# Kernel optimization log

Measured on AMD Instinct MI355X. Metric: run time of the kernel, lower is better.

Reference implementation:

```python
import jax, jax.numpy as jnp
from jax import lax
import numpy as np

# db3 analysis/synthesis filter bank (pywt coefficients)
DEC_LO = np.array([0.035226291882100656, -0.085441273882241486, -0.13501102001039084,
                   0.45987750211933132, 0.80689150931333875, 0.33267055295095688], dtype=np.float32)
DEC_HI = np.array([-0.33267055295095688, 0.80689150931333875, -0.45987750211933132,
                   -0.13501102001039084, 0.085441273882241486, 0.035226291882100656], dtype=np.float32)
REC_LO = DEC_LO[::-1].copy()
REC_HI = np.array([0.035226291882100656, 0.085441273882241486, -0.13501102001039084,
                   -0.45987750211933132, 0.80689150931333875, -0.33267055295095688], dtype=np.float32)
L = 6  # db3 filter length
DN = ('NCHW', 'OIHW', 'NCHW')

# analysis correlation kernels (torch conv2d correlates, pytorch_wavelets pre-flips dec filters)
H0_A = jnp.asarray(DEC_LO[::-1].copy())
H1_A = jnp.asarray(DEC_HI[::-1].copy())
# synthesis: conv_transpose(x, g, stride=2, pad=L-2) == correlate(dilate(x,2), flip(g), pad=1)
G0_S = jnp.asarray(REC_LO[::-1].copy())
G1_S = jnp.asarray(REC_HI[::-1].copy())


def _sep_conv(x, f, axis, stride=1, lhs_dil=1, pad=0):
    """Depthwise 1-D correlation along H (axis=2) or W (axis=3) of an NCHW tensor."""
    C = x.shape[1]
    if axis == 2:
        k = jnp.tile(f.reshape(1, 1, -1, 1), (C, 1, 1, 1))
        strides, dil, padding = (stride, 1), (lhs_dil, 1), ((pad, pad), (0, 0))
    else:
        k = jnp.tile(f.reshape(1, 1, 1, -1), (C, 1, 1, 1))
        strides, dil, padding = (1, stride), (1, lhs_dil), ((0, 0), (pad, pad))
    return lax.conv_general_dilated(x, k, strides, padding, lhs_dilation=dil,
                                    dimension_numbers=DN, feature_group_count=C)


def _dwt2(x):
    # single-level separable 2D DWT, mode='zero' (pytorch_wavelets: rows then cols)
    lo = _sep_conv(x, H0_A, 3, stride=2, pad=L - 2)
    hi = _sep_conv(x, H1_A, 3, stride=2, pad=L - 2)
    ll = _sep_conv(lo, H0_A, 2, stride=2, pad=L - 2)
    lh = _sep_conv(lo, H1_A, 2, stride=2, pad=L - 2)  # yh[:,:,0]
    hl = _sep_conv(hi, H0_A, 2, stride=2, pad=L - 2)  # yh[:,:,1]
    hh = _sep_conv(hi, H1_A, 2, stride=2, pad=L - 2)  # yh[:,:,2]
    return ll, lh, hl, hh


def _idwt2(ll, lh, hl, hh):
    # inverse: cols then rows; transposed conv realized as lhs_dilation=2 + pad 1
    lo = _sep_conv(ll, G0_S, 2, lhs_dil=2, pad=1) + _sep_conv(lh, G1_S, 2, lhs_dil=2, pad=1)
    hi = _sep_conv(hl, G0_S, 2, lhs_dil=2, pad=1) + _sep_conv(hh, G1_S, 2, lhs_dil=2, pad=1)
    return _sep_conv(lo, G0_S, 3, lhs_dil=2, pad=1) + _sep_conv(hi, G1_S, 3, lhs_dil=2, pad=1)


def _dw3x3(x, w):
    # depthwise 3x3, padding 1, no bias; w: (C,1,3,3)
    return lax.conv_general_dilated(x, w, (1, 1), ((1, 1), (1, 1)),
                                    dimension_numbers=DN, feature_group_count=x.shape[1])


def _ssl(x, conv5_w, conv7_w, conv9_w):
    # faithful to original: conv5 applied to BOTH yl and ylh; conv1/conv_cat unused
    ll, lh, hl, hh = _dwt2(x)
    return _idwt2(_dw3x3(ll, conv5_w), _dw3x3(lh, conv5_w),
                  _dw3x3(hl, conv7_w), _dw3x3(hh, conv9_w))


def setup_inputs() -> dict:
    key = jax.random.key(0)
    ks = jax.random.split(key, 7)
    B, C, H, W, HEADS = 4, 256, 192, 192, 8
    s = 0.05
    return {
        'x': jax.random.normal(ks[0], (B, C, H, W), jnp.float32),
        'qkv_w': jax.random.normal(ks[1], (2 * C, C), jnp.float32) * s,        # 1x1 conv C->2C
        'qkv_conv_w': jax.random.normal(ks[2], (2 * C, 1, 3, 3), jnp.float32) * s,  # depthwise 3x3
        'conv5_w': jax.random.normal(ks[3], (C, 1, 3, 3), jnp.float32) * s,
        'conv7_w': jax.random.normal(ks[4], (C, 1, 3, 3), jnp.float32) * s,
        'conv9_w': jax.random.normal(ks[5], (C, 1, 3, 3), jnp.float32) * s,
        'proj_w': jax.random.normal(ks[6], (C, C), jnp.float32) * s,           # 1x1 conv C->C
        'temperature': jnp.ones((1, HEADS, 1, 1), jnp.float32),
        'num_heads': HEADS,
    }


def reference(x, qkv_w, qkv_conv_w, conv5_w, conv7_w, conv9_w, proj_w, temperature, num_heads):
    b, c, h, w = x.shape
    eps = 1e-12
    kv = jnp.einsum('oc,bchw->bohw', qkv_w, x)          # 1x1 conv, no bias
    kv = _dw3x3(kv, qkv_conv_w)
    k, v = jnp.split(kv, 2, axis=1)
    q = _ssl(x, conv5_w, conv7_w, conv9_w)              # wavelet query path, same HxW
    d = c // num_heads
    q = q.reshape(b, num_heads, d, h * w)
    k = k.reshape(b, num_heads, d, h * w)
    v = v.reshape(b, num_heads, d, h * w)
    q = q / jnp.maximum(jnp.linalg.norm(q, axis=-1, keepdims=True), eps)
    k = k / jnp.maximum(jnp.linalg.norm(k, axis=-1, keepdims=True), eps)
    attn = jax.nn.softmax(jnp.einsum('bhdn,bhen->bhde', q, k) * temperature, axis=-1)  # (b,H,d,d)
    out = jnp.einsum('bhde,bhen->bhdn', attn, v).reshape(b, c, h, w)
    return jnp.einsum('oc,bchw->bohw', proj_w, out)
```

## Files before the change

### kernel.cpp

```cpp
#include <hip/hip_runtime.h>
#include <hip/hip_bf16.h>

typedef __hip_bfloat16 bf16;
typedef __attribute__((ext_vector_type(8))) short short8v;
typedef __attribute__((ext_vector_type(4))) float f32x4;

#define NB 4
#define NC 256
#define NPIX 36864
#define NH 192
#define NW 192
#define SW 98
#define SH 98
#define SUBN 9604
#define PSUB 9834496
#define GCH 24

__device__ __constant__ float cH0A[6] = {  0.33267055295095688f,  0.80689150931333875f,  0.45987750211933132f, -0.13501102001039084f, -0.085441273882241486f, 0.035226291882100656f };
__device__ __constant__ float cH1A[6] = {  0.035226291882100656f, 0.085441273882241486f, -0.13501102001039084f, -0.45987750211933132f,  0.80689150931333875f, -0.33267055295095688f };
__device__ __constant__ float cG0S[6] = {  0.035226291882100656f, -0.085441273882241486f, -0.13501102001039084f, 0.45987750211933132f,  0.80689150931333875f,  0.33267055295095688f };
__device__ __constant__ float cG1S[6] = { -0.33267055295095688f,  0.80689150931333875f, -0.45987750211933132f, -0.13501102001039084f,  0.085441273882241486f, 0.035226291882100656f };

__device__ inline unsigned short bfbits(float f) {
    bf16 h = __float2bfloat16(f);
    return *reinterpret_cast<unsigned short*>(&h);
}
__device__ inline float b2f(short s) {
    return __bfloat162float(*reinterpret_cast<const bf16*>(&s));
}

__global__ __launch_bounds__(256) void k_dwt(const float* __restrict__ x, bf16* __restrict__ sub) {
    int band = blockIdx.x;
    int bc = blockIdx.y;
    int ho0 = band * 14;
    int jbase = 2 * ho0 - 4;
    __shared__ float s_x[32][192];
    __shared__ float s_lo[32][100];
    __shared__ float s_hi[32][100];
    const float* xp = x + (size_t)bc * NPIX;
    int t = threadIdx.x;
#pragma unroll
    for (int i = 0; i < 8; ++i) {
        int e = t + 256 * i;
        int row = e >> 6, c4 = e & 63;
        if (c4 < 48) {
            int jg = jbase + row;
            float4 v = make_float4(0.f, 0.f, 0.f, 0.f);
            if (jg >= 0 && jg < NH) v = *reinterpret_cast<const float4*>(xp + (size_t)jg * NW + c4 * 4);
            *reinterpret_cast<float4*>(&s_x[row][c4 * 4]) = v;
        }
    }
    __syncthreads();
#pragma unroll
    for (int i = 0; i < 16; ++i) {
        int e = t + 256 * i;
        int r = e >> 7, wo = e & 127;
        if (wo < 98) {
            int basec = 2 * wo - 4;
            float la = 0.f, ha = 0.f;
#pragma unroll
            for (int tp = 0; tp < 6; ++tp) {
                int j = basec + tp;
                if (j >= 0 && j < NW) {
                    float v = s_x[r][j];
                    la = fmaf(v, cH0A[tp], la);
                    ha = fmaf(v, cH1A[tp], ha);
                }
            }
            s_lo[r][wo] = la; s_hi[r][wo] = ha;
        }
    }
    __syncthreads();
    bf16* sp = sub + (size_t)bc * SUBN;
#pragma unroll
    for (int i = 0; i < 7; ++i) {
        int e = t + 256 * i;
        int ho = e >> 7, wo = e & 127;
        if (wo < 98) {
            float ll = 0.f, lh = 0.f, hl = 0.f, hh = 0.f;
#pragma unroll
            for (int tp = 0; tp < 6; ++tp) {
                float lv = s_lo[2 * ho + tp][wo];
                float hv = s_hi[2 * ho + tp][wo];
                ll = fmaf(lv, cH0A[tp], ll); lh = fmaf(lv, cH1A[tp], lh);
                hl = fmaf(hv, cH0A[tp], hl); hh = fmaf(hv, cH1A[tp], hh);
            }
            size_t o = (size_t)(ho0 + ho) * SW + wo;
            sp[o] = __float2bfloat16(ll);
            sp[(size_t)PSUB + o] = __float2bfloat16(lh);
            sp[2 * (size_t)PSUB + o] = __float2bfloat16(hl);
            sp[3 * (size_t)PSUB + o] = __float2bfloat16(hh);
        }
    }
}

__global__ __launch_bounds__(256) void k_synth2(const bf16* __restrict__ sub,
                                                const float* __restrict__ w5, const float* __restrict__ w7,
                                                const float* __restrict__ w9,
                                                bf16* __restrict__ q, float* __restrict__ qsum) {
    int w0 = blockIdx.x * 64, h0 = blockIdx.y * 32;
    int bc = blockIdx.z;
    int c = bc & 255;
    int jh0 = h0 >> 1, jw0 = w0 >> 1;
    __shared__ short s_sub[4][20][38];
    __shared__ float s_c[4][18][34];
    __shared__ float s_lh[2][32][34];
    __shared__ float s_w[4][9];
    __shared__ float red[4];
    const bf16* sp = sub + (size_t)bc * SUBN;
    int t = threadIdx.x;
    if (t < 36) {
        int f = t / 9, k = t - f * 9;
        const float* wsel = (f <= 1) ? w5 : (f == 2 ? w7 : w9);
        s_w[f][k] = wsel[c * 9 + k];
    }
    for (int e = t; e < 1520; e += 256) {
        int pl = e / 380;
        int r2 = e - pl * 380;
        int r = r2 / 19, j = r2 - r * 19;
        int gr = jh0 - 1 + r;
        int gc = jw0 - 2 + 2 * j;
        ushort2 u = make_ushort2(0, 0);
        if (gr >= 0 && gr < SH && gc >= 0 && gc < 97)
            u = *reinterpret_cast<const ushort2*>(sp + (size_t)pl * PSUB + (size_t)gr * SW + gc);
        *reinterpret_cast<ushort2*>(&s_sub[pl][r][2 * j]) = u;
    }
    float ge0[3] = { cG0S[1], cG0S[3], cG0S[5] };
    float go0[3] = { cG0S[0], cG0S[2], cG0S[4] };
    float ge1[3] = { cG1S[1], cG1S[3], cG1S[5] };
    float go1[3] = { cG1S[0], cG1S[2], cG1S[4] };
    __syncthreads();
    for (int e = t; e < 2448; e += 256) {
        int pl = e / 612;
        int r2 = e - pl * 612;
        int r = r2 / 34, cc = r2 - r * 34;
        const float* wp = s_w[pl];
        float a = 0.f;
#pragma unroll
        for (int ky = 0; ky < 3; ++ky)
#pragma unroll
            for (int kx = 0; kx < 3; ++kx)
                a = fmaf(b2f(s_sub[pl][r + ky][cc + 1 + kx]), wp[ky * 3 + kx], a);
        s_c[pl][r][cc] = a;
    }
    __syncthreads();
    for (int e = t; e < 2176; e += 256) {
        int which = e / 1088;
        int r2 = e - which * 1088;
        int hh = r2 / 34, cc = r2 - hh * 34;
        int par = hh & 1;
        int j0 = hh >> 1;
        float a = 0.f;
#pragma unroll
        for (int i = 0; i < 3; ++i) {
            float g0 = par ? go0[i] : ge0[i];
            float g1 = par ? go1[i] : ge1[i];
            a = fmaf(s_c[2 * which][j0 + i][cc], g0, a);
            a = fmaf(s_c[2 * which + 1][j0 + i][cc], g1, a);
        }
        s_lh[which][hh][cc] = a;
    }
    __syncthreads();
    float lsum = 0.f;
    bf16* qp = q + (size_t)bc * NPIX;
#pragma unroll
    for (int it = 0; it < 8; ++it) {
        int e = t + 256 * it;
        int hh = e >> 6, ww = e & 63;
        int par = ww & 1;
        int j0 = ww >> 1;
        float a = 0.f;
#pragma unroll
        for (int i = 0; i < 3; ++i) {
            float g0 = par ? go0[i] : ge0[i];
            float g1 = par ? go1[i] : ge1[i];
            a = fmaf(s_lh[0][hh][j0 + i], g0, a);
            a = fmaf(s_lh[1][hh][j0 + i], g1, a);
        }
        qp[(size_t)(h0 + hh) * NW + w0 + ww] = __float2bfloat16(a);
        lsum = fmaf(a, a, lsum);
    }
#pragma unroll
    for (int off = 32; off; off >>= 1) lsum += __shfl_down(lsum, off, 64);
    if ((t & 63) == 0) red[t >> 6] = lsum;
    __syncthreads();
    if (t == 0) atomicAdd(&qsum[bc], red[0] + red[1] + red[2] + red[3]);
}

__global__ __launch_bounds__(256) void k_xpose(const float* __restrict__ x, bf16* __restrict__ xT) {
    __shared__ float T[64][68];
    int nt = blockIdx.x, ct = blockIdx.y, b = blockIdx.z;
    int n0 = nt * 64, c0 = ct * 64;
    const float* xb = x + ((size_t)b * NC + c0) * NPIX + n0;
    int t = threadIdx.x;
    int tr = t >> 4, tc4 = (t & 15) * 4;
#pragma unroll
    for (int i = 0; i < 4; ++i) {
        int cc = tr + i * 16;
        float4 v = *reinterpret_cast<const float4*>(xb + (size_t)cc * NPIX + tc4);
        T[cc][tc4] = v.x; T[cc][tc4 + 1] = v.y; T[cc][tc4 + 2] = v.z; T[cc][tc4 + 3] = v.w;
    }
    __syncthreads();
    bf16* ob = xT + ((size_t)b * NPIX + n0) * NC + c0;
#pragma unroll
    for (int i = 0; i < 4; ++i) {
        int nn = tr + i * 16;
        ushort4 u;
        u.x = bfbits(T[tc4][nn]); u.y = bfbits(T[tc4 + 1][nn]);
        u.z = bfbits(T[tc4 + 2][nn]); u.w = bfbits(T[tc4 + 3][nn]);
        *reinterpret_cast<ushort4*>(ob + (size_t)nn * NC + tc4) = u;
    }
}

__global__ __launch_bounds__(256) void k_cvtw(const float* __restrict__ w, bf16* __restrict__ wb) {
    int idx = blockIdx.x * 256 + threadIdx.x;
    if (idx < 512 * 256) wb[idx] = __float2bfloat16(w[idx]);
}

template <typename TOUT>
__global__ __launch_bounds__(256) void k_gemm_bf(const bf16* __restrict__ X, const bf16* __restrict__ Wm,
                                                 int wStride, TOUT* __restrict__ Out) {
    __shared__ __align__(16) short As[128 * 64];
    __shared__ __align__(16) short Bs[128 * 64];
    int nt = blockIdx.x, ot = blockIdx.y, b = blockIdx.z;
    int n0 = nt * 128, o0 = ot * 128;
    const bf16* xb = X + (size_t)b * NPIX * NC;
    const bf16* Wb = Wm + (size_t)b * wStride;
    int t = threadIdx.x;
    int wv = t >> 6, l = t & 63;
    int wr = wv >> 1, wc = wv & 1;
    f32x4 z4 = {0.f, 0.f, 0.f, 0.f};
    f32x4 acc[4][4];
#pragma unroll
    for (int m = 0; m < 4; ++m)
#pragma unroll
        for (int nf = 0; nf < 4; ++nf) acc[m][nf] = z4;
    for (int kc = 0; kc < 256; kc += 64) {
        __syncthreads();
#pragma unroll
        for (int i = 0; i < 4; ++i) {
            int blk = t + 256 * i;
            int r = blk >> 3, cb = blk & 7;
            int cbs = cb ^ (r & 7);
            *(short8v*)(As + r * 64 + cbs * 8) = *(const short8v*)(Wb + (size_t)(o0 + r) * NC + kc + cb * 8);
            *(short8v*)(Bs + r * 64 + cbs * 8) = *(const short8v*)(xb + (size_t)(n0 + r) * NC + kc + cb * 8);
        }
        __syncthreads();
#pragma unroll
        for (int kk = 0; kk < 2; ++kk) {
            int col8 = kk * 4 + (l >> 4);
            short8v av[4], bv[4];
#pragma unroll
            for (int m = 0; m < 4; ++m) {
                int row = wr * 64 + m * 16 + (l & 15);
                av[m] = *(const short8v*)(As + row * 64 + (col8 ^ (row & 7)) * 8);
            }
#pragma unroll
            for (int nf = 0; nf < 4; ++nf) {
                int row = wc * 64 + nf * 16 + (l & 15);
                bv[nf] = *(const short8v*)(Bs + row * 64 + (col8 ^ (row & 7)) * 8);
            }
#pragma unroll
            for (int m = 0; m < 4; ++m)
#pragma unroll
                for (int nf = 0; nf < 4; ++nf)
                    acc[m][nf] = __builtin_amdgcn_mfma_f32_16x16x32_bf16(av[m], bv[nf], acc[m][nf], 0, 0, 0);
        }
    }
    TOUT* ob = Out + (size_t)b * NC * NPIX;
#pragma unroll
    for (int m = 0; m < 4; ++m)
#pragma unroll
        for (int nf = 0; nf < 4; ++nf)
#pragma unroll
            for (int r = 0; r < 4; ++r) {
                int oo = o0 + wr * 64 + m * 16 + (l >> 4) * 4 + r;
                int nn = n0 + wc * 64 + nf * 16 + (l & 15);
                if constexpr (sizeof(TOUT) == 2)
                    ob[(size_t)oo * NPIX + nn] = __float2bfloat16(acc[m][nf][r]);
                else
                    ob[(size_t)oo * NPIX + nn] = acc[m][nf][r];
            }
}

__device__ inline short8v dw8(const bf16* __restrict__ chan, int r, int cb,
                              const float* __restrict__ w, float& ks) {
    float v[3][10];
#pragma unroll
    for (int ri = 0; ri < 3; ++ri) {
        int r2 = r + ri - 1;
        if (r2 < 0 || r2 >= NH) {
#pragma unroll
            for (int j = 0; j < 10; ++j) v[ri][j] = 0.f;
        } else {
            const bf16* p = chan + (size_t)r2 * NW + cb;
            short8v m = *(const short8v*)p;
            v[ri][0] = (cb > 0) ? __bfloat162float(p[-1]) : 0.f;
#pragma unroll
            for (int j = 0; j < 8; ++j) v[ri][j + 1] = b2f(m[j]);
            v[ri][9] = (cb < 184) ? __bfloat162float(p[8]) : 0.f;
        }
    }
    short8v out;
#pragma unroll
    for (int j = 0; j < 8; ++j) {
        float a = 0.f;
#pragma unroll
        for (int ri = 0; ri < 3; ++ri) {
            a = fmaf(v[ri][j],     w[ri * 3 + 0], a);
            a = fmaf(v[ri][j + 1], w[ri * 3 + 1], a);
            a = fmaf(v[ri][j + 2], w[ri * 3 + 2], a);
        }
        ks = fmaf(a, a, ks);
        out[j] = (short)bfbits(a);
    }
    return out;
}

__global__ __launch_bounds__(256) void k_gram_dw(const bf16* __restrict__ qbf, const bf16* __restrict__ kraw,
                                                 const float* __restrict__ dwW,
                                                 float* __restrict__ gpart, float* __restrict__ ksum) {
    int chunk = blockIdx.x;
    int bh = blockIdx.y; int b = bh >> 3, h = bh & 7;
    const bf16* qb = qbf + ((size_t)b * NC + h * 32) * NPIX;
    const bf16* kb = kraw + ((size_t)b * NC + h * 32) * NPIX;
    __shared__ float sg[4][1024];
    __shared__ float ksh[32];
    int t = threadIdx.x;
    int wv = t >> 6, l = t & 63;
    int dlo = l & 15, kslot = l >> 4;
    float wA[9], wB[9];
#pragma unroll
    for (int i = 0; i < 9; ++i) {
        wA[i] = dwW[(h * 32 + dlo) * 9 + i];
        wB[i] = dwW[(h * 32 + dlo + 16) * 9 + i];
    }
    const bf16* q0 = qb + (size_t)dlo * NPIX;
    const bf16* q1 = qb + (size_t)(dlo + 16) * NPIX;
    const bf16* k0 = kb + (size_t)dlo * NPIX;
    const bf16* k1 = kb + (size_t)(dlo + 16) * NPIX;
    f32x4 z4 = {0.f, 0.f, 0.f, 0.f};
    f32x4 a00 = z4, a01 = z4, a10 = z4, a11 = z4;
    float ks0 = 0.f, ks1 = 0.f;
    int r0 = chunk * 8 + wv * 2;
#pragma unroll
    for (int rr = 0; rr < 2; ++rr) {
        int r = r0 + rr;
#pragma unroll
        for (int c0 = 0; c0 < 192; c0 += 32) {
            int cb = c0 + kslot * 8;
            short8v av0 = *(const short8v*)(q0 + (size_t)r * NW + cb);
            short8v av1 = *(const short8v*)(q1 + (size_t)r * NW + cb);
            short8v bv0 = dw8(k0, r, cb, wA, ks0);
            short8v bv1 = dw8(k1, r, cb, wB, ks1);
            a00 = __builtin_amdgcn_mfma_f32_16x16x32_bf16(av0, bv0, a00, 0, 0, 0);
            a01 = __builtin_amdgcn_mfma_f32_16x16x32_bf16(av0, bv1, a01, 0, 0, 0);
            a10 = __builtin_amdgcn_mfma_f32_16x16x32_bf16(av1, bv0, a10, 0, 0, 0);
            a11 = __builtin_amdgcn_mfma_f32_16x16x32_bf16(av1, bv1, a11, 0, 0, 0);
        }
    }
    if (t < 32) ksh[t] = 0.f;
#pragma unroll
    for (int j = 0; j < 4; ++j) {
        int dA = kslot * 4 + j, dB = 16 + kslot * 4 + j;
        sg[wv][dA * 32 + dlo]      = a00[j];
        sg[wv][dA * 32 + 16 + dlo] = a01[j];
        sg[wv][dB * 32 + dlo]      = a10[j];
        sg[wv][dB * 32 + 16 + dlo] = a11[j];
    }
    __syncthreads();
    float* gp = gpart + ((size_t)bh * GCH + chunk) * 1024;
#pragma unroll
    for (int i = 0; i < 4; ++i) {
        int e = t + 256 * i;
        gp[e] = sg[0][e] + sg[1][e] + sg[2][e] + sg[3][e];
    }
    atomicAdd(&ksh[dlo], ks0);
    atomicAdd(&ksh[dlo + 16], ks1);
    __syncthreads();
    if (t < 32) atomicAdd(&ksum[b * NC + h * 32 + t], ksh[t]);
}

__global__ __launch_bounds__(1024) void k_attn(const float* __restrict__ gpart, const float* __restrict__ qsum,
                                               const float* __restrict__ ksum, const float* __restrict__ temp,
                                               float* __restrict__ attn) {
    int bh = blockIdx.x;
    int b = bh >> 3, h = bh & 7;
    int t = threadIdx.x;
    int d = t >> 5, e = t & 31;
    float s = 0.f;
    for (int i = 0; i < GCH; ++i) s += gpart[((size_t)bh * GCH + i) * 1024 + t];
    float rq = 1.f / fmaxf(sqrtf(qsum[b * NC + h * 32 + d]), 1e-12f);
    float rk = 1.f / fmaxf(sqrtf(ksum[b * NC + h * 32 + e]), 1e-12f);
    s *= rq * rk * temp[h];
    float m = s;
#pragma unroll
    for (int off = 16; off; off >>= 1) m = fmaxf(m, __shfl_xor(m, off, 32));
    float ex = expf(s - m);
    float sum = ex;
#pragma unroll
    for (int off = 16; off; off >>= 1) sum += __shfl_xor(sum, off, 32);
    attn[(size_t)bh * 1024 + t] = ex / sum;
}

__global__ __launch_bounds__(256) void k_wfold(const float* __restrict__ proj, const float* __restrict__ attn,
                                               bf16* __restrict__ wfbf) {
    int o = blockIdx.x, b = blockIdx.y;
    int t = threadIdx.x;
    int h = t >> 5, e = t & 31;
    const float* ap = attn + (size_t)(b * 8 + h) * 1024 + e;
    const float* pp = proj + o * NC + h * 32;
    float acc = 0.f;
#pragma unroll
    for (int d = 0; d < 32; ++d) acc = fmaf(pp[d], ap[d * 32], acc);
    wfbf[((size_t)b * NC + o) * NC + t] = __float2bfloat16(acc);
}

__global__ __launch_bounds__(256) void k_dwv(const bf16* __restrict__ vraw, const float* __restrict__ dwW,
                                             bf16* __restrict__ v2T) {
    int r = blockIdx.x;
    int cg = blockIdx.y;
    int b = blockIdx.z;
    __shared__ short s_v[3][32][204];
    const bf16* vb = vraw + ((size_t)b * NC + cg * 32) * NPIX;
    int t = threadIdx.x;
    for (int idx = t; idx < 4800; idx += 256) {
        int ri = idx / 1600;
        int rem = idx - ri * 1600;
        int e = rem / 50, j = rem - e * 50;
        int gr = r + ri - 1;
        int gc0 = -4 + 4 * j;
        ushort4 u = make_ushort4(0, 0, 0, 0);
        if (gr >= 0 && gr < NH && gc0 >= 0 && gc0 + 3 < NW)
            u = *reinterpret_cast<const ushort4*>(vb + (size_t)e * NPIX + (size_t)gr * NW + gc0);
        *reinterpret_cast<ushort4*>(&s_v[ri][e][4 * j]) = u;
    }
    int e = t & 31;
    int wslot = t >> 5;
    float w9[9];
#pragma unroll
    for (int i = 0; i < 9; ++i) w9[i] = dwW[(256 + cg * 32 + e) * 9 + i];
    __syncthreads();
    bf16* ob = v2T + ((size_t)b * NPIX + (size_t)r * NW) * NC + cg * 32 + e;
#pragma unroll
    for (int wi = 0; wi < 24; ++wi) {
        int w = wslot + 8 * wi;
        int cbase = w + 3;
        float a = 0.f;
#pragma unroll
        for (int ri = 0; ri < 3; ++ri) {
            a = fmaf(b2f(s_v[ri][e][cbase]),     w9[ri * 3 + 0], a);
            a = fmaf(b2f(s_v[ri][e][cbase + 1]), w9[ri * 3 + 1], a);
            a = fmaf(b2f(s_v[ri][e][cbase + 2]), w9[ri * 3 + 2], a);
        }
        ob[(size_t)w * NC] = __float2bfloat16(a);
    }
}


extern "C" void kernel_launch(void* const* d_in, const int* in_sizes, int n_in,
                              void* d_out, int out_size, void* d_ws, size_t ws_size,
                              hipStream_t stream) {
    (void)in_sizes; (void)n_in; (void)out_size;
    const float* x      = (const float*)d_in[0];
    const float* qkv_w  = (const float*)d_in[1];
    const float* qkv_cw = (const float*)d_in[2];
    const float* w5     = (const float*)d_in[3];
    const float* w7     = (const float*)d_in[4];
    const float* w9     = (const float*)d_in[5];
    const float* projw  = (const float*)d_in[6];
    const float* temp   = (const float*)d_in[7];

    const size_t OFF_SM    = 78675968;
    const size_t OFF_WBF   = OFF_SM;
    const size_t OFF_QSUM  = OFF_SM + 262144;
    const size_t OFF_KSUM  = OFF_QSUM + 4096;
    const size_t OFF_GPART = OFF_KSUM + 4096;
    const size_t OFF_ATTN  = OFF_GPART + 3145728;
    const size_t OFF_WF    = OFF_ATTN + 131072;
    const size_t WS_NEED   = OFF_WF + 524288;
    if (ws_size < WS_NEED) return;

    char* ws = (char*)d_ws;
    bf16*  sub   = (bf16*)ws;
    bf16*  kraw  = (bf16*)ws;
    bf16*  v2T   = (bf16*)ws;
    bf16*  wbf   = (bf16*)(ws + OFF_WBF);
    float* qsum  = (float*)(ws + OFF_QSUM);
    float* ksum  = (float*)(ws + OFF_KSUM);
    float* gpart = (float*)(ws + OFF_GPART);
    float* attn  = (float*)(ws + OFF_ATTN);
    bf16*  wfbf  = (bf16*)(ws + OFF_WF);

    bf16*  xbf  = (bf16*)d_out;
    bf16*  qbf  = (bf16*)((char*)d_out + 75497472);
    bf16*  vraw = (bf16*)((char*)d_out + 75497472);
    float* out  = (float*)d_out;

    hipMemsetAsync(ws + OFF_QSUM, 0, 8192, stream);

    k_dwt<<<dim3(7, NB * NC), 256, 0, stream>>>(x, sub);
    k_synth2<<<dim3(3, 6, NB * NC), 256, 0, stream>>>(sub, w5, w7, w9, qbf, qsum);

    k_xpose<<<dim3(576, 4, NB), 256, 0, stream>>>(x, xbf);
    k_cvtw<<<512, 256, 0, stream>>>(qkv_w, wbf);

    k_gemm_bf<bf16><<<dim3(288, 2, NB), 256, 0, stream>>>(xbf, wbf, 0, kraw);
    k_gram_dw<<<dim3(GCH, 32), 256, 0, stream>>>(qbf, kraw, qkv_cw, gpart, ksum);

    k_attn<<<32, 1024, 0, stream>>>(gpart, qsum, ksum, temp, attn);
    k_wfold<<<dim3(256, NB), 256, 0, stream>>>(projw, attn, wfbf);

    k_gemm_bf<bf16><<<dim3(288, 2, NB), 256, 0, stream>>>(xbf, wbf + 256 * 256, 0, vraw);
    k_dwv<<<dim3(NH, 8, NB), 256, 0, stream>>>(vraw, qkv_cw, v2T);
    k_gemm_bf<float><<<dim3(288, 2, NB), 256, 0, stream>>>(v2T, wfbf, 65536, out);
}
```

Measured before the change: 621.7 us.

## Fuse DWT analysis into synthesis kernel, recomputing subbands per tile with halo

Removes the separate k_dwt kernel and its global bf16 subband buffer. The synthesis kernel now loads an x tile with halo, runs row and column analysis filters in shared memory, and builds the subband tile it needs directly. This drops a kernel launch and the global write and read of the four subband planes. In exchange, overlapping halos are recomputed, shared memory use per block grows, and intermediate lo/hi values are rounded to bf16, a numerical change.

```diff
diff --git a/kernel.cpp b/kernel.cpp
--- a/kernel.cpp
+++ b/kernel.cpp
@@ -12,8 +12,6 @@
 #define NW 192
 #define SW 98
 #define SH 98
-#define SUBN 9604
-#define PSUB 9834496
 #define GCH 24
 
 __device__ __constant__ float cH0A[6] = {  0.33267055295095688f,  0.80689150931333875f,  0.45987750211933132f, -0.13501102001039084f, -0.085441273882241486f, 0.035226291882100656f };
@@ -28,102 +26,82 @@
 __device__ inline float b2f(short s) {
     return __bfloat162float(*reinterpret_cast<const bf16*>(&s));
 }
-
-__global__ __launch_bounds__(256) void k_dwt(const float* __restrict__ x, bf16* __restrict__ sub) {
-    int band = blockIdx.x;
-    int bc = blockIdx.y;
-    int ho0 = band * 14;
-    int jbase = 2 * ho0 - 4;
-    __shared__ float s_x[32][192];
-    __shared__ float s_lo[32][100];
-    __shared__ float s_hi[32][100];
-    const float* xp = x + (size_t)bc * NPIX;
-    int t = threadIdx.x;
-#pragma unroll
-    for (int i = 0; i < 8; ++i) {
-        int e = t + 256 * i;
-        int row = e >> 6, c4 = e & 63;
-        if (c4 < 48) {
-            int jg = jbase + row;
-            float4 v = make_float4(0.f, 0.f, 0.f, 0.f);
-            if (jg >= 0 && jg < NH) v = *reinterpret_cast<const float4*>(xp + (size_t)jg * NW + c4 * 4);
-            *reinterpret_cast<float4*>(&s_x[row][c4 * 4]) = v;
-        }
-    }
-    __syncthreads();
-#pragma unroll
-    for (int i = 0; i < 16; ++i) {
-        int e = t + 256 * i;
-        int r = e >> 7, wo = e & 127;
-        if (wo < 98) {
-            int basec = 2 * wo - 4;
-            float la = 0.f, ha = 0.f;
-#pragma unroll
-            for (int tp = 0; tp < 6; ++tp) {
-                int j = basec + tp;
-                if (j >= 0 && j < NW) {
-                    float v = s_x[r][j];
-                    la = fmaf(v, cH0A[tp], la);
-                    ha = fmaf(v, cH1A[tp], ha);
-                }
-            }
-            s_lo[r][wo] = la; s_hi[r][wo] = ha;
-        }
-    }
-    __syncthreads();
-    bf16* sp = sub + (size_t)bc * SUBN;
-#pragma unroll
-    for (int i = 0; i < 7; ++i) {
-        int e = t + 256 * i;
-        int ho = e >> 7, wo = e & 127;
-        if (wo < 98) {
-            float ll = 0.f, lh = 0.f, hl = 0.f, hh = 0.f;
-#pragma unroll
-            for (int tp = 0; tp < 6; ++tp) {
-                float lv = s_lo[2 * ho + tp][wo];
-                float hv = s_hi[2 * ho + tp][wo];
-                ll = fmaf(lv, cH0A[tp], ll); lh = fmaf(lv, cH1A[tp], lh);
-                hl = fmaf(hv, cH0A[tp], hl); hh = fmaf(hv, cH1A[tp], hh);
-            }
-            size_t o = (size_t)(ho0 + ho) * SW + wo;
-            sp[o] = __float2bfloat16(ll);
-            sp[(size_t)PSUB + o] = __float2bfloat16(lh);
-            sp[2 * (size_t)PSUB + o] = __float2bfloat16(hl);
-            sp[3 * (size_t)PSUB + o] = __float2bfloat16(hh);
-        }
-    }
-}
-
-__global__ __launch_bounds__(256) void k_synth2(const bf16* __restrict__ sub,
-                                                const float* __restrict__ w5, const float* __restrict__ w7,
-                                                const float* __restrict__ w9,
-                                                bf16* __restrict__ q, float* __restrict__ qsum) {
+__device__ inline short f2s(float f) {
+    bf16 h = __float2bfloat16(f);
+    return *reinterpret_cast<short*>(&h);
+}
+
+__global__ __launch_bounds__(256) void k_wave(const float* __restrict__ x,
+                                              const float* __restrict__ w5, const float* __restrict__ w7,
+                                              const float* __restrict__ w9,
+                                              bf16* __restrict__ q, float* __restrict__ qsum) {
     int w0 = blockIdx.x * 64, h0 = blockIdx.y * 32;
     int bc = blockIdx.z;
     int c = bc & 255;
     int jh0 = h0 >> 1, jw0 = w0 >> 1;
+    int xr0 = 2 * jh0 - 6;
+    int xc0 = 2 * jw0 - 8;
+    __shared__ float s_x[44][80];
+    __shared__ short s_lo[44][38];
+    __shared__ short s_hi[44][38];
     __shared__ short s_sub[4][20][38];
     __shared__ float s_c[4][18][34];
     __shared__ float s_lh[2][32][34];
     __shared__ float s_w[4][9];
     __shared__ float red[4];
-    const bf16* sp = sub + (size_t)bc * SUBN;
+    const float* xp = x + (size_t)bc * NPIX;
     int t = threadIdx.x;
     if (t < 36) {
         int f = t / 9, k = t - f * 9;
         const float* wsel = (f <= 1) ? w5 : (f == 2 ? w7 : w9);
         s_w[f][k] = wsel[c * 9 + k];
     }
-    for (int e = t; e < 1520; e += 256) {
-        int pl = e / 380;
-        int r2 = e - pl * 380;
-        int r = r2 / 19, j = r2 - r * 19;
-        int gr = jh0 - 1 + r;
-        int gc = jw0 - 2 + 2 * j;
-        ushort2 u = make_ushort2(0, 0);
-        if (gr >= 0 && gr < SH && gc >= 0 && gc < 97)
-            u = *reinterpret_cast<const ushort2*>(sp + (size_t)pl * PSUB + (size_t)gr * SW + gc);
-        *reinterpret_cast<ushort2*>(&s_sub[pl][r][2 * j]) = u;
+    for (int e = t; e < 880; e += 256) {
+        int r = e / 20, s = e - r * 20;
+        int row = xr0 + r, col0 = xc0 + s * 4;
+        float4 v = make_float4(0.f, 0.f, 0.f, 0.f);
+        if (row >= 0 && row < NH) {
+            if (col0 >= 0 && col0 + 3 < NW) {
+                v = *reinterpret_cast<const float4*>(xp + (size_t)row * NW + col0);
+            } else {
+#pragma unroll
+                for (int j = 0; j < 4; ++j) {
+                    int cc = col0 + j;
+                    if (cc >= 0 && cc < NW) (&v.x)[j] = xp[(size_t)row * NW + cc];
+                }
+            }
+        }
+        *reinterpret_cast<float4*>(&s_x[r][s * 4]) = v;
+    }
+    __syncthreads();
+    for (int e = t; e < 1672; e += 256) {
+        int r = e / 38, jc = e - r * 38;
+        float la = 0.f, ha = 0.f;
+#pragma unroll
+        for (int tp = 0; tp < 6; ++tp) {
+            float v = s_x[r][2 * jc + tp];
+            la = fmaf(v, cH0A[tp], la);
+            ha = fmaf(v, cH1A[tp], ha);
+        }
+        s_lo[r][jc] = f2s(la); s_hi[r][jc] = f2s(ha);
+    }
+    __syncthreads();
+    for (int e = t; e < 760; e += 256) {
+        int r = e / 38, jc = e - r * 38;
+        int gr = jh0 - 1 + r, gcol = jw0 - 2 + jc;
+        bool inb = (gr >= 0 && gr < SH && gcol >= 0 && gcol < SW);
+        float ll = 0.f, lh = 0.f, hl = 0.f, hh = 0.f;
+#pragma unroll
+        for (int tp = 0; tp < 6; ++tp) {
+            float lv = b2f(s_lo[2 * r + tp][jc]);
+            float hv = b2f(s_hi[2 * r + tp][jc]);
+            ll = fmaf(lv, cH0A[tp], ll); lh = fmaf(lv, cH1A[tp], lh);
+            hl = fmaf(hv, cH0A[tp], hl); hh = fmaf(hv, cH1A[tp], hh);
+        }
+        s_sub[0][r][jc] = inb ? f2s(ll) : (short)0;
+        s_sub[1][r][jc] = inb ? f2s(lh) : (short)0;
+        s_sub[2][r][jc] = inb ? f2s(hl) : (short)0;
+        s_sub[3][r][jc] = inb ? f2s(hh) : (short)0;
     }
     float ge0[3] = { cG0S[1], cG0S[3], cG0S[5] };
     float go0[3] = { cG0S[0], cG0S[2], cG0S[4] };
@@ -482,7 +460,6 @@
     if (ws_size < WS_NEED) return;
 
     char* ws = (char*)d_ws;
-    bf16*  sub   = (bf16*)ws;
     bf16*  kraw  = (bf16*)ws;
     bf16*  v2T   = (bf16*)ws;
     bf16*  wbf   = (bf16*)(ws + OFF_WBF);
@@ -499,8 +476,7 @@
 
     hipMemsetAsync(ws + OFF_QSUM, 0, 8192, stream);
 
-    k_dwt<<<dim3(7, NB * NC), 256, 0, stream>>>(x, sub);
-    k_synth2<<<dim3(3, 6, NB * NC), 256, 0, stream>>>(sub, w5, w7, w9, qbf, qsum);
+    k_wave<<<dim3(3, 6, NB * NC), 256, 0, stream>>>(x, w5, w7, w9, qbf, qsum);
 
     k_xpose<<<dim3(576, 4, NB), 256, 0, stream>>>(x, xbf);
     k_cvtw<<<512, 256, 0, stream>>>(qkv_w, wbf);
```

Result: faster. 594.3 us (-4.4%).
